# Optimization experiments

Hardware: AMD Instinct MI355X
Metric: run time of the kernel (lower is better)

## Reference

```python
import jax, jax.numpy as jnp
import numpy as np

B, T, C, H = 8, 2048, 1024, 64  # batch, seq_len(block_size), embedding_size, head_size


def setup_inputs() -> dict:
    key = jax.random.key(0)
    kx, kk, kq, kv = jax.random.split(key, 4)
    x = jax.random.normal(kx, (B, T, C), dtype=jnp.float32)
    # nn.Linear(C, H, bias=False) weights, stored as [in, out] for x @ W
    s = 1.0 / np.sqrt(C)
    Wk = jax.random.uniform(kk, (C, H), dtype=jnp.float32, minval=-s, maxval=s)
    Wq = jax.random.uniform(kq, (C, H), dtype=jnp.float32, minval=-s, maxval=s)
    Wv = jax.random.uniform(kv, (C, H), dtype=jnp.float32, minval=-s, maxval=s)
    return {"x": x, "Wk": Wk, "Wq": Wq, "Wv": Wv}


def reference(x, Wk, Wq, Wv):
    Bx, Tx, Cx = x.shape
    k = jnp.einsum('btc,ch->bth', x, Wk)
    q = jnp.einsum('btc,ch->bth', x, Wq)
    v = jnp.einsum('btc,ch->bth', x, Wv)
    # NOTE: original scales by embedding dim C ** -0.5, not head_size
    scores = jnp.einsum('bth,bsh->bts', q, k) * (Cx ** -0.5)  # [B,T,T]
    causal = jnp.tril(jnp.ones((Tx, Tx), dtype=bool))
    scores = jnp.where(causal, scores, -jnp.inf)
    attn = jax.nn.softmax(scores, axis=-1)
    # dropout is identity in eval/deterministic mode
    out = jnp.einsum('bts,bsh->bth', attn, v)  # [B,T,H]
    return out
```

## Files before the change

kernel.cpp:

```cpp
#include <hip/hip_runtime.h>
#include <hip/hip_bf16.h>
#include <math.h>


#define BT 16384
#define TSEQ 2048
#define XST 72

typedef __attribute__((ext_vector_type(8))) __bf16 bf16x8;
typedef __attribute__((ext_vector_type(8))) unsigned short ushort8;
typedef __attribute__((ext_vector_type(4))) float floatx4;

#define MFMA16(a, b, c) __builtin_amdgcn_mfma_f32_16x16x32_bf16( \
    __builtin_bit_cast(bf16x8, (a)), __builtin_bit_cast(bf16x8, (b)), (c), 0, 0, 0)

__device__ inline unsigned short f2bf(float f) {
  unsigned u = __builtin_bit_cast(unsigned, f);
  u += 0x7FFFu + ((u >> 16) & 1u);
  return (unsigned short)(u >> 16);
}
__device__ inline float bf2f(unsigned short s) {
  return __builtin_bit_cast(float, (unsigned)s << 16);
}
__device__ inline unsigned long long pack4bf(floatx4 f) {
  return (unsigned long long)f2bf(f[0]) | ((unsigned long long)f2bf(f[1]) << 16) |
         ((unsigned long long)f2bf(f[2]) << 32) | ((unsigned long long)f2bf(f[3]) << 48);
}
__device__ inline ushort8 pack8bf(floatx4 a, floatx4 b) {
  ushort8 t;
#pragma unroll
  for (int i = 0; i < 4; ++i) t[i] = f2bf(a[i]);
#pragma unroll
  for (int i = 0; i < 4; ++i) t[4 + i] = f2bf(b[i]);
  return t;
}
__device__ inline void glds16(const unsigned short* g, unsigned short* l) {
  __builtin_amdgcn_global_load_lds(
      (const __attribute__((address_space(1))) unsigned int*)g,
      (__attribute__((address_space(3))) unsigned int*)l, 16, 0, 0);
}

__global__ __launch_bounds__(256) void wt2_kernel(
    const float* __restrict__ Wq, const float* __restrict__ Wk,
    const float* __restrict__ Wv, unsigned short* __restrict__ Wt2) {
  __shared__ float ls[64][65];
  const int m = blockIdx.x >> 4;
  const int kci = blockIdx.x & 15;
  const int c0 = kci << 6;
  const float* __restrict__ W = (m == 0) ? Wq : (m == 1) ? Wk : Wv;
  const int tid = threadIdx.x;
#pragma unroll
  for (int i = 0; i < 16; ++i) {
    int idx = tid + (i << 8);
    int cl = idx >> 6, h = idx & 63;
    ls[cl][h] = W[(c0 + cl) * 64 + h];
  }
  __syncthreads();
  const int w = tid >> 6, lane = tid & 63;
  const int quad = lane >> 4, l16 = lane & 15;
  const int nt = (m << 2) + w;
#pragma unroll
  for (int half = 0; half < 2; ++half) {
    ushort8 t;
#pragma unroll
    for (int j = 0; j < 8; ++j)
      t[j] = f2bf(ls[(half << 5) + (quad << 3) + j][(w << 4) + l16]);
    *(ushort8*)(Wt2 + ((size_t)(((nt << 4) + kci) * 2 + half) << 9) +
                (lane << 3)) = t;
  }
}

#define XBS 4608
#define BB0 9216
#define BBS 12288

__global__ __launch_bounds__(512) void qkv_mfma(
    const float* __restrict__ x, const unsigned short* __restrict__ Wt2,
    unsigned short* __restrict__ Qf, unsigned short* __restrict__ Kf,
    unsigned short* __restrict__ Vf) {
  __shared__ __align__(16) unsigned short smem[46080];

  const int tid = threadIdx.x;
  const int w = tid >> 6, lane = tid & 63;
  const int quad = lane >> 4, l16 = lane & 15;
  const int wr = w >> 2, wn = w & 3;
  const int r0 = blockIdx.x << 6;
  const int xrow = (w << 3) + (lane >> 3);
  const int xcol = (lane & 7) << 3;
  const float* __restrict__ xp = x + (size_t)(r0 + xrow) * 1024 + xcol;
  const int xw_u16 = xrow * XST + xcol;

  floatx4 acc[2][3];
#pragma unroll
  for (int rt = 0; rt < 2; ++rt)
#pragma unroll
    for (int n = 0; n < 3; ++n) acc[rt][n] = (floatx4){0.f, 0.f, 0.f, 0.f};

  floatx4 pf[2][2];
  pf[0][0] = *(const floatx4*)(xp);
  pf[0][1] = *(const floatx4*)(xp + 4);
  __builtin_amdgcn_sched_barrier(0);
#pragma unroll
  for (int i = 0; i < 3; ++i) {
    const int f = 3 * w + i;
    glds16(Wt2 + ((size_t)(((f >> 1) << 4) * 2 + (f & 1)) << 9) + (lane << 3),
           &smem[BB0 + (f << 9)]);
  }
  __builtin_amdgcn_sched_barrier(0);
  pf[1][0] = *(const floatx4*)(xp + 64);
  pf[1][1] = *(const floatx4*)(xp + 68);
  __builtin_amdgcn_sched_barrier(0);
#pragma unroll
  for (int i = 0; i < 3; ++i) {
    const int f = 3 * w + i;
    glds16(Wt2 + ((size_t)((((f >> 1) << 4) + 1) * 2 + (f & 1)) << 9) +
               (lane << 3),
           &smem[BB0 + BBS + (f << 9)]);
  }
  __builtin_amdgcn_sched_barrier(0);
  *(ushort8*)&smem[xw_u16] = pack8bf(pf[0][0], pf[0][1]);
  __builtin_amdgcn_sched_barrier(0);
  asm volatile("s_waitcnt vmcnt(5)");
  asm volatile("s_waitcnt lgkmcnt(0)");
  __builtin_amdgcn_sched_barrier(0);
  __builtin_amdgcn_s_barrier();
  __builtin_amdgcn_sched_barrier(0);

#pragma unroll
  for (int c = 0; c < 16; ++c) {
    if (c + 1 < 16)
      *(ushort8*)&smem[((c + 1) & 1) * XBS + xw_u16] =
          pack8bf(pf[(c + 1) & 1][0], pf[(c + 1) & 1][1]);
    __builtin_amdgcn_sched_barrier(0);
    if (c + 2 < 16) {
      pf[c & 1][0] = *(const floatx4*)(xp + ((c + 2) << 6));
      pf[c & 1][1] = *(const floatx4*)(xp + ((c + 2) << 6) + 4);
      __builtin_amdgcn_sched_barrier(0);
#pragma unroll
      for (int i = 0; i < 3; ++i) {
        const int f = 3 * w + i;
        glds16(Wt2 + ((size_t)((((f >> 1) << 4) + (c + 2)) * 2 + (f & 1)) << 9) +
                   (lane << 3),
               &smem[BB0 + ((c + 2) % 3) * BBS + (f << 9)]);
      }
    }
    __builtin_amdgcn_sched_barrier(0);

    ushort8 af[2][2];
#pragma unroll
    for (int rt = 0; rt < 2; ++rt)
#pragma unroll
      for (int h = 0; h < 2; ++h)
        af[rt][h] = *(const ushort8*)&smem[(c & 1) * XBS +
            ((wr << 5) + (rt << 4) + l16) * XST + (h << 5) + (quad << 3)];
    ushort8 bfr[3][2];
#pragma unroll
    for (int n = 0; n < 3; ++n)
#pragma unroll
      for (int h = 0; h < 2; ++h)
        bfr[n][h] = *(const ushort8*)&smem[BB0 + (c % 3) * BBS +
            ((((3 * wn + n) << 1) + h) << 9) + (lane << 3)];
#pragma unroll
    for (int h = 0; h < 2; ++h)
#pragma unroll
      for (int rt = 0; rt < 2; ++rt)
#pragma unroll
        for (int n = 0; n < 3; ++n)
          acc[rt][n] = MFMA16(af[rt][h], bfr[n][h], acc[rt][n]);

    __builtin_amdgcn_sched_barrier(0);
    if (c < 14) { asm volatile("s_waitcnt vmcnt(5)"); }
    else        { asm volatile("s_waitcnt vmcnt(0)"); }
    asm volatile("s_waitcnt lgkmcnt(0)");
    __builtin_amdgcn_sched_barrier(0);
    __builtin_amdgcn_s_barrier();
    __builtin_amdgcn_sched_barrier(0);
  }

#pragma unroll
  for (int n = 0; n < 3; ++n) {
    const int nt = 3 * wn + n;
    const int m = nt >> 2, hg = nt & 3;
#pragma unroll
    for (int rt = 0; rt < 2; ++rt) {
      const int rowb = (wr << 5) + (rt << 4) + (quad << 2);
      if (m < 2) {
#pragma unroll
        for (int r = 0; r < 4; ++r)
          smem[m * XBS + (rowb + r) * XST + (hg << 4) + l16] =
              f2bf(acc[rt][n][r]);
      } else {
        *(unsigned long long*)&smem[2 * XBS + ((hg << 4) + l16) * XST + rowb] =
            pack4bf(acc[rt][n]);
      }
    }
  }
  __syncthreads();

  const int b = blockIdx.x >> 5, st = blockIdx.x & 31;
#pragma unroll
  for (int i = 0; i < 3; ++i) {
    const int f = w * 3 + i;
    const int m = f >> 3, idx = f & 7, grp = idx >> 1, kh = idx & 1;
    ushort8 t = *(const ushort8*)&smem[m * XBS + ((grp << 4) + l16) * XST +
                                       (kh << 5) + (quad << 3)];
    unsigned short* dst;
    if (m == 0)
      dst = Qf + (((size_t)(b * 128 + (st << 2) + grp) * 2 + kh) << 9);
    else if (m == 1)
      dst = Kf + (((size_t)((b * 32 + st) * 4 + grp) * 2 + kh) << 9);
    else
      dst = Vf + (((size_t)((b * 32 + st) * 4 + grp) * 2 + kh) << 9);
    *(ushort8*)(dst + (lane << 3)) = t;
  }
}

__global__ __launch_bounds__(256, 3) void attn_part(
    const unsigned short* __restrict__ Qf, const unsigned short* __restrict__ Kf,
    const unsigned short* __restrict__ Vf, float* __restrict__ part) {
  __shared__ __align__(16) unsigned short KV[2][8192];
  __shared__ unsigned short Pw[4][16 * XST];

  const int tid = threadIdx.x;
  const int w = tid >> 6, lane = tid & 63;
  const int quad = lane >> 4, l16 = lane & 15;
  const int b = blockIdx.x / 144;
  const int e = blockIdx.x - b * 144;
  int g = 0;
#pragma unroll
  for (int gg = 1; gg < 8; ++gg) g += (e >= 2 * gg * (gg + 1)) ? 1 : 0;
  const int rem2 = e - 2 * g * (g + 1);
  const int qt = (g << 2) + rem2 / (g + 1);
  const int ch = rem2 - (rem2 / (g + 1)) * (g + 1);
  const int s0 = ch << 2;
  const int s1 = (s0 + 4 < qt + 1) ? s0 + 4 : qt + 1;
  const int r16 = (qt << 2) + w;

#define KVIDX(ss, nt, kh) \
  (((((size_t)(b * 32 + (ss)) << 2) + (nt)) * 2 + (kh)) << 9)
#define STAGE_KV(ss, db)                                                     \
  {                                                                          \
    _Pragma("unroll") for (int r_ = 0; r_ < 4; ++r_) {                       \
      const int f_ = (r_ << 2) + w;                                          \
      const unsigned short* src_ =                                           \
          (f_ < 8) ? Kf + KVIDX(ss, (f_ >> 1), (f_ & 1)) + (lane << 3)       \
                   : Vf + KVIDX(ss, (f_ >> 1) - 4, (f_ & 1)) + (lane << 3);  \
      glds16(src_, &KV[db][f_ << 9]);                                        \
    }                                                                        \
  }

  const unsigned short* qbase =
      Qf + ((((size_t)b * 128 + r16) * 2) << 9) + (lane << 3);
  ushort8 qf0 = *(const ushort8*)qbase;
  ushort8 qf1 = *(const ushort8*)(qbase + 512);
  __builtin_amdgcn_sched_barrier(0);

  STAGE_KV(s0, 0);
  __builtin_amdgcn_sched_barrier(0);
  STAGE_KV((s0 + 1 < s1) ? s0 + 1 : s1 - 1, 1);
  __builtin_amdgcn_sched_barrier(0);
  asm volatile("s_waitcnt vmcnt(4)");
  __builtin_amdgcn_sched_barrier(0);
  __builtin_amdgcn_s_barrier();
  __builtin_amdgcn_sched_barrier(0);

  floatx4 acc[4], lacc;
#pragma unroll
  for (int nt = 0; nt < 4; ++nt) acc[nt] = (floatx4){0.f, 0.f, 0.f, 0.f};
  lacc = (floatx4){0.f, 0.f, 0.f, 0.f};
  const ushort8 ones = {0x3F80, 0x3F80, 0x3F80, 0x3F80,
                        0x3F80, 0x3F80, 0x3F80, 0x3F80};

  for (int s = s0; s < s1; ++s) {
    const int cur = (s - s0) & 1;
    ushort8 bk[4][2], bv[4][2];
#pragma unroll
    for (int nt = 0; nt < 4; ++nt)
#pragma unroll
      for (int kh = 0; kh < 2; ++kh) {
        bk[nt][kh] = *(const ushort8*)&KV[cur][((((nt << 1) + kh)) << 9) +
                                              (lane << 3)];
        bv[nt][kh] = *(const ushort8*)&KV[cur][(((8 + (nt << 1) + kh)) << 9) +
                                              (lane << 3)];
      }
    asm volatile("s_waitcnt lgkmcnt(0)");
    __builtin_amdgcn_sched_barrier(0);
    __builtin_amdgcn_s_barrier();
    __builtin_amdgcn_sched_barrier(0);

    STAGE_KV((s + 2 < s1) ? s + 2 : s1 - 1, cur);
    __builtin_amdgcn_sched_barrier(0);

    floatx4 sf[4];
#pragma unroll
    for (int nt = 0; nt < 4; ++nt) {
      sf[nt] = (floatx4){0.f, 0.f, 0.f, 0.f};
      sf[nt] = MFMA16(qf0, bk[nt][0], sf[nt]);
      sf[nt] = MFMA16(qf1, bk[nt][1], sf[nt]);
    }

    const bool diag = (s == qt);
    const int qrow = (w << 4) + (quad << 2);
#pragma unroll
    for (int nt = 0; nt < 4; ++nt) {
      const int keyl = (nt << 4) + l16;
#pragma unroll
      for (int r = 0; r < 4; ++r) {
        float ev = __expf(sf[nt][r] * 0.03125f);
        if (diag && keyl > qrow + r) ev = 0.f;
        Pw[w][((quad << 2) + r) * XST + keyl] = f2bf(ev);
      }
    }

#pragma unroll
    for (int kh = 0; kh < 2; ++kh) {
      ushort8 pa = *(const ushort8*)&Pw[w][l16 * XST + (kh << 5) + (quad << 3)];
      lacc = MFMA16(pa, ones, lacc);
#pragma unroll
      for (int nt = 0; nt < 4; ++nt) acc[nt] = MFMA16(pa, bv[nt][kh], acc[nt]);
    }

    __builtin_amdgcn_sched_barrier(0);
    asm volatile("s_waitcnt vmcnt(4)");
    __builtin_amdgcn_sched_barrier(0);
    __builtin_amdgcn_s_barrier();
    __builtin_amdgcn_sched_barrier(0);
  }
#undef STAGE_KV
#undef KVIDX

  float* slot = part + (size_t)(b * 144 + e) * 2112;
  if (l16 == 0) {
#pragma unroll
    for (int r = 0; r < 4; ++r) slot[(w << 4) + (quad << 2) + r] = lacc[r];
  }
  unsigned short* op = (unsigned short*)(slot + 64);
#pragma unroll
  for (int nt = 0; nt < 4; ++nt)
#pragma unroll
    for (int r = 0; r < 4; ++r)
      op[((w << 4) + (quad << 2) + r) * 64 + (nt << 4) + l16] = f2bf(acc[nt][r]);
}

__global__ __launch_bounds__(256) void attn_combine(
    const float* __restrict__ part, float* __restrict__ out) {
  const int rh = blockIdx.x & 1;
  const int bqt = blockIdx.x >> 1;
  const int b = bqt >> 5, qt = bqt & 31;
  const int tid = threadIdx.x;
  const int row = (rh << 5) + (tid >> 3);
  const int hseg = (tid & 7) << 3;
  const int g = qt >> 2;
  const int nch = g + 1;
  const int ebase = 2 * g * (g + 1) + (qt & 3) * (g + 1);

  float l = 0.f;
  float ov[8];
#pragma unroll
  for (int i = 0; i < 8; ++i) ov[i] = 0.f;
  for (int c = 0; c < nch; ++c) {
    const float* slot = part + (size_t)(b * 144 + ebase + c) * 2112;
    l += slot[row];
    ushort8 o0 = *(const ushort8*)((const unsigned short*)(slot + 64) +
                                   row * 64 + hseg);
#pragma unroll
    for (int i = 0; i < 8; ++i) ov[i] += bf2f(o0[i]);
  }
  const float inv = 1.f / l;
  float* o = out + ((size_t)(b * TSEQ + (qt << 6) + row)) * 64 + hseg;
#pragma unroll
  for (int i = 0; i < 8; ++i) o[i] = ov[i] * inv;
}

extern "C" void kernel_launch(void* const* d_in, const int* in_sizes, int n_in,
                              void* d_out, int out_size, void* d_ws, size_t ws_size,
                              hipStream_t stream) {
  const float* x  = (const float*)d_in[0];
  const float* Wk = (const float*)d_in[1];
  const float* Wq = (const float*)d_in[2];
  const float* Wv = (const float*)d_in[3];

  unsigned short* Qfw = (unsigned short*)d_ws;
  unsigned short* Kfw = Qfw + (size_t)BT * 64;
  unsigned short* Vfw = Kfw + (size_t)BT * 64;
  unsigned short* Wt2 = Vfw + (size_t)BT * 64;
  float* part = (float*)(Wt2 + 3 * 64 * 1024);

  wt2_kernel<<<48, 256, 0, stream>>>(Wq, Wk, Wv, Wt2);
  qkv_mfma<<<256, 512, 0, stream>>>(x, Wt2, Qfw, Kfw, Vfw);
  attn_part<<<1152, 256, 0, stream>>>(Qfw, Kfw, Vfw, part);
  attn_combine<<<512, 256, 0, stream>>>(part, (float*)d_out);
}
```

Measured before the change: 130.7 us.

## Shrink QKV projection tiles to 16 rows and load weights directly into registers

The QKV projection kernel moves from 64-row tiles on 256 blocks of 512 threads to 16-row tiles on 1024 blocks of 256 threads. Weight fragments are now loaded straight from global memory into registers and double-buffered, instead of being staged through LDS with global_load_lds. LDS use drops sharply and occupancy rises, so the 256 CUs get more work and latency is hidden better. In exchange, each weight fragment is reloaded by four times as many blocks, which raises L2 traffic, and the V-transpose store path becomes more complicated.

```diff
diff --git a/kernel.cpp b/kernel.cpp
--- a/kernel.cpp
+++ b/kernel.cpp
@@ -25,14 +25,6 @@
 __device__ inline unsigned long long pack4bf(floatx4 f) {
   return (unsigned long long)f2bf(f[0]) | ((unsigned long long)f2bf(f[1]) << 16) |
          ((unsigned long long)f2bf(f[2]) << 32) | ((unsigned long long)f2bf(f[3]) << 48);
-}
-__device__ inline ushort8 pack8bf(floatx4 a, floatx4 b) {
-  ushort8 t;
-#pragma unroll
-  for (int i = 0; i < 4; ++i) t[i] = f2bf(a[i]);
-#pragma unroll
-  for (int i = 0; i < 4; ++i) t[4 + i] = f2bf(b[i]);
-  return t;
 }
 __device__ inline void glds16(const unsigned short* g, unsigned short* l) {
   __builtin_amdgcn_global_load_lds(
@@ -70,148 +62,121 @@
   }
 }
 
-#define XBS 4608
-#define BB0 9216
-#define BBS 12288
-
-__global__ __launch_bounds__(512) void qkv_mfma(
+#define XB16 1152
+
+__global__ __launch_bounds__(256, 4) void qkv_mfma(
     const float* __restrict__ x, const unsigned short* __restrict__ Wt2,
     unsigned short* __restrict__ Qf, unsigned short* __restrict__ Kf,
     unsigned short* __restrict__ Vf) {
-  __shared__ __align__(16) unsigned short smem[46080];
+  __shared__ __align__(16) unsigned short smem[3840];
 
   const int tid = threadIdx.x;
   const int w = tid >> 6, lane = tid & 63;
   const int quad = lane >> 4, l16 = lane & 15;
-  const int wr = w >> 2, wn = w & 3;
-  const int r0 = blockIdx.x << 6;
-  const int xrow = (w << 3) + (lane >> 3);
-  const int xcol = (lane & 7) << 3;
+  const int r0 = blockIdx.x << 4;
+  const int xrow = tid >> 4;
+  const int xcol = (tid & 15) << 2;
   const float* __restrict__ xp = x + (size_t)(r0 + xrow) * 1024 + xcol;
-  const int xw_u16 = xrow * XST + xcol;
-
-  floatx4 acc[2][3];
-#pragma unroll
-  for (int rt = 0; rt < 2; ++rt)
-#pragma unroll
-    for (int n = 0; n < 3; ++n) acc[rt][n] = (floatx4){0.f, 0.f, 0.f, 0.f};
-
-  floatx4 pf[2][2];
-  pf[0][0] = *(const floatx4*)(xp);
-  pf[0][1] = *(const floatx4*)(xp + 4);
-  __builtin_amdgcn_sched_barrier(0);
+  const int xw = xrow * XST + xcol;
+  const unsigned short* __restrict__ bbase = Wt2 + (lane << 3);
+
+  floatx4 acc[3];
+#pragma unroll
+  for (int n = 0; n < 3; ++n) acc[n] = (floatx4){0.f, 0.f, 0.f, 0.f};
+
+  floatx4 pf[4];
+#pragma unroll
+  for (int s = 0; s < 4; ++s) pf[s] = *(const floatx4*)(xp + (s << 6));
+  ushort8 bfr[2][3][2];
+#pragma unroll
+  for (int n = 0; n < 3; ++n)
+#pragma unroll
+    for (int h = 0; h < 2; ++h)
+      bfr[0][n][h] = *(const ushort8*)(bbase +
+          ((size_t)(((3 * w + n) << 5) + h) << 9));
+  *(unsigned long long*)&smem[xw] = pack4bf(pf[0]);
+  asm volatile("s_waitcnt lgkmcnt(0)" ::: "memory");
+  __builtin_amdgcn_sched_barrier(0);
+  __builtin_amdgcn_s_barrier();
+  __builtin_amdgcn_sched_barrier(0);
+
+#pragma unroll
+  for (int c = 0; c < 16; ++c) {
+    const int cur = c & 1;
+    if (c + 1 < 16)
+      *(unsigned long long*)&smem[((c + 1) & 1) * XB16 + xw] =
+          pack4bf(pf[(c + 1) & 3]);
+    if (c + 4 < 16) pf[c & 3] = *(const floatx4*)(xp + ((c + 4) << 6));
+    if (c + 1 < 16) {
+#pragma unroll
+      for (int n = 0; n < 3; ++n)
+#pragma unroll
+        for (int h = 0; h < 2; ++h)
+          bfr[(c + 1) & 1][n][h] = *(const ushort8*)(bbase +
+              ((size_t)((((3 * w + n) << 4) + (c + 1)) * 2 + h) << 9));
+    }
+    ushort8 af[2];
+#pragma unroll
+    for (int h = 0; h < 2; ++h)
+      af[h] = *(const ushort8*)&smem[cur * XB16 + l16 * XST + (h << 5) +
+                                     (quad << 3)];
+#pragma unroll
+    for (int h = 0; h < 2; ++h)
+#pragma unroll
+      for (int n = 0; n < 3; ++n)
+        acc[n] = MFMA16(af[h], bfr[cur][n][h], acc[n]);
+
+    asm volatile("s_waitcnt lgkmcnt(0)" ::: "memory");
+    __builtin_amdgcn_sched_barrier(0);
+    __builtin_amdgcn_s_barrier();
+    __builtin_amdgcn_sched_barrier(0);
+  }
+
 #pragma unroll
   for (int i = 0; i < 3; ++i) {
-    const int f = 3 * w + i;
-    glds16(Wt2 + ((size_t)(((f >> 1) << 4) * 2 + (f & 1)) << 9) + (lane << 3),
-           &smem[BB0 + (f << 9)]);
-  }
-  __builtin_amdgcn_sched_barrier(0);
-  pf[1][0] = *(const floatx4*)(xp + 64);
-  pf[1][1] = *(const floatx4*)(xp + 68);
-  __builtin_amdgcn_sched_barrier(0);
-#pragma unroll
-  for (int i = 0; i < 3; ++i) {
-    const int f = 3 * w + i;
-    glds16(Wt2 + ((size_t)((((f >> 1) << 4) + 1) * 2 + (f & 1)) << 9) +
-               (lane << 3),
-           &smem[BB0 + BBS + (f << 9)]);
-  }
-  __builtin_amdgcn_sched_barrier(0);
-  *(ushort8*)&smem[xw_u16] = pack8bf(pf[0][0], pf[0][1]);
-  __builtin_amdgcn_sched_barrier(0);
-  asm volatile("s_waitcnt vmcnt(5)");
-  asm volatile("s_waitcnt lgkmcnt(0)");
-  __builtin_amdgcn_sched_barrier(0);
-  __builtin_amdgcn_s_barrier();
-  __builtin_amdgcn_sched_barrier(0);
-
-#pragma unroll
-  for (int c = 0; c < 16; ++c) {
-    if (c + 1 < 16)
-      *(ushort8*)&smem[((c + 1) & 1) * XBS + xw_u16] =
-          pack8bf(pf[(c + 1) & 1][0], pf[(c + 1) & 1][1]);
-    __builtin_amdgcn_sched_barrier(0);
-    if (c + 2 < 16) {
-      pf[c & 1][0] = *(const floatx4*)(xp + ((c + 2) << 6));
-      pf[c & 1][1] = *(const floatx4*)(xp + ((c + 2) << 6) + 4);
-      __builtin_amdgcn_sched_barrier(0);
-#pragma unroll
-      for (int i = 0; i < 3; ++i) {
-        const int f = 3 * w + i;
-        glds16(Wt2 + ((size_t)((((f >> 1) << 4) + (c + 2)) * 2 + (f & 1)) << 9) +
-                   (lane << 3),
-               &smem[BB0 + ((c + 2) % 3) * BBS + (f << 9)]);
+    const int nt = 3 * w + i;
+    const int m = nt >> 2, hg = nt & 3;
+    if (m < 2) {
+#pragma unroll
+      for (int r = 0; r < 4; ++r)
+        smem[m * XB16 + ((quad << 2) + r) * XST + (hg << 4) + l16] =
+            f2bf(acc[i][r]);
+    } else {
+      *(unsigned long long*)&smem[2304 + ((hg << 4) + l16) * 24 + (quad << 2)] =
+          pack4bf(acc[i]);
+    }
+  }
+  __syncthreads();
+
+  const int b = r0 >> 11;
+  const int r16 = (r0 & 2047) >> 4;
+  const int st = (r0 & 2047) >> 6;
+  const int ntK = (r0 >> 4) & 3;
+  const int khV = (r0 >> 5) & 1;
+  const int q0v = (r0 >> 3) & 3;
+#pragma unroll
+  for (int i = 0; i < 2; ++i) {
+    const int f = (w << 1) + i;
+    if (f < 2) {
+      const int kh = f;
+      ushort8 t = *(const ushort8*)&smem[l16 * XST + (kh << 5) + (quad << 3)];
+      *(ushort8*)(Qf + ((((size_t)b * 128 + r16) * 2 + kh) << 9) +
+                  (lane << 3)) = t;
+    } else if (f < 4) {
+      const int kh = f - 2;
+      ushort8 t = *(const ushort8*)&smem[XB16 + l16 * XST + (kh << 5) +
+                                         (quad << 3)];
+      *(ushort8*)(Kf + ((((size_t)(b * 32 + st) * 4 + ntK) * 2 + kh) << 9) +
+                  (lane << 3)) = t;
+    } else {
+      const int ntE = f - 4;
+      if ((quad >> 1) == (q0v >> 1)) {
+        ushort8 t = *(const ushort8*)&smem[2304 + ((ntE << 4) + l16) * 24 +
+                                           ((quad - q0v) << 3)];
+        *(ushort8*)(Vf + ((((size_t)(b * 32 + st) * 4 + ntE) * 2 + khV) << 9) +
+                    (lane << 3)) = t;
       }
     }
-    __builtin_amdgcn_sched_barrier(0);
-
-    ushort8 af[2][2];
-#pragma unroll
-    for (int rt = 0; rt < 2; ++rt)
-#pragma unroll
-      for (int h = 0; h < 2; ++h)
-        af[rt][h] = *(const ushort8*)&smem[(c & 1) * XBS +
-            ((wr << 5) + (rt << 4) + l16) * XST + (h << 5) + (quad << 3)];
-    ushort8 bfr[3][2];
-#pragma unroll
-    for (int n = 0; n < 3; ++n)
-#pragma unroll
-      for (int h = 0; h < 2; ++h)
-        bfr[n][h] = *(const ushort8*)&smem[BB0 + (c % 3) * BBS +
-            ((((3 * wn + n) << 1) + h) << 9) + (lane << 3)];
-#pragma unroll
-    for (int h = 0; h < 2; ++h)
-#pragma unroll
-      for (int rt = 0; rt < 2; ++rt)
-#pragma unroll
-        for (int n = 0; n < 3; ++n)
-          acc[rt][n] = MFMA16(af[rt][h], bfr[n][h], acc[rt][n]);
-
-    __builtin_amdgcn_sched_barrier(0);
-    if (c < 14) { asm volatile("s_waitcnt vmcnt(5)"); }
-    else        { asm volatile("s_waitcnt vmcnt(0)"); }
-    asm volatile("s_waitcnt lgkmcnt(0)");
-    __builtin_amdgcn_sched_barrier(0);
-    __builtin_amdgcn_s_barrier();
-    __builtin_amdgcn_sched_barrier(0);
-  }
-
-#pragma unroll
-  for (int n = 0; n < 3; ++n) {
-    const int nt = 3 * wn + n;
-    const int m = nt >> 2, hg = nt & 3;
-#pragma unroll
-    for (int rt = 0; rt < 2; ++rt) {
-      const int rowb = (wr << 5) + (rt << 4) + (quad << 2);
-      if (m < 2) {
-#pragma unroll
-        for (int r = 0; r < 4; ++r)
-          smem[m * XBS + (rowb + r) * XST + (hg << 4) + l16] =
-              f2bf(acc[rt][n][r]);
-      } else {
-        *(unsigned long long*)&smem[2 * XBS + ((hg << 4) + l16) * XST + rowb] =
-            pack4bf(acc[rt][n]);
-      }
-    }
-  }
-  __syncthreads();
-
-  const int b = blockIdx.x >> 5, st = blockIdx.x & 31;
-#pragma unroll
-  for (int i = 0; i < 3; ++i) {
-    const int f = w * 3 + i;
-    const int m = f >> 3, idx = f & 7, grp = idx >> 1, kh = idx & 1;
-    ushort8 t = *(const ushort8*)&smem[m * XBS + ((grp << 4) + l16) * XST +
-                                       (kh << 5) + (quad << 3)];
-    unsigned short* dst;
-    if (m == 0)
-      dst = Qf + (((size_t)(b * 128 + (st << 2) + grp) * 2 + kh) << 9);
-    else if (m == 1)
-      dst = Kf + (((size_t)((b * 32 + st) * 4 + grp) * 2 + kh) << 9);
-    else
-      dst = Vf + (((size_t)((b * 32 + st) * 4 + grp) * 2 + kh) << 9);
-    *(ushort8*)(dst + (lane << 3)) = t;
   }
 }
 
@@ -387,7 +352,7 @@
   float* part = (float*)(Wt2 + 3 * 64 * 1024);
 
   wt2_kernel<<<48, 256, 0, stream>>>(Wq, Wk, Wv, Wt2);
-  qkv_mfma<<<256, 512, 0, stream>>>(x, Wt2, Qfw, Kfw, Vfw);
+  qkv_mfma<<<1024, 256, 0, stream>>>(x, Wt2, Qfw, Kfw, Vfw);
   attn_part<<<1152, 256, 0, stream>>>(Qfw, Kfw, Vfw, part);
   attn_combine<<<512, 256, 0, stream>>>(part, (float*)d_out);
 }
```

Result: slower. 139.8 us (+7.0%).

## Split QKV projection into per-matrix blocks with XCD-aware row grouping

Applied to the files above, without the earlier changes.

The QKV projection kernel now launches 768 blocks of 256 threads instead of 256 blocks of 512, with each block computing only one of Q, K or V for a 64-row tile. Block indices are remapped so the three blocks sharing an x row tile land on the same XCD, which should help L2 reuse of x. This gives more blocks for occupancy across CUs and a smaller LDS footprint, and the x prefetch pipeline deepens to three stages. The cost is that each x tile is read from global memory three times instead of once.

```diff
diff --git a/kernel.cpp b/kernel.cpp
--- a/kernel.cpp
+++ b/kernel.cpp
@@ -70,57 +70,63 @@
   }
 }
 
-#define XBS 4608
-#define BB0 9216
-#define BBS 12288
-
-__global__ __launch_bounds__(512) void qkv_mfma(
+#define XQB 4608
+#define BQ0 9216
+#define BQS 4096
+
+__global__ __launch_bounds__(256, 3) void qkv_mfma(
     const float* __restrict__ x, const unsigned short* __restrict__ Wt2,
     unsigned short* __restrict__ Qf, unsigned short* __restrict__ Kf,
     unsigned short* __restrict__ Vf) {
-  __shared__ __align__(16) unsigned short smem[46080];
+  __shared__ __align__(16) unsigned short smem[21504];
 
   const int tid = threadIdx.x;
   const int w = tid >> 6, lane = tid & 63;
   const int quad = lane >> 4, l16 = lane & 15;
-  const int wr = w >> 2, wn = w & 3;
-  const int r0 = blockIdx.x << 6;
-  const int xrow = (w << 3) + (lane >> 3);
-  const int xcol = (lane & 7) << 3;
-  const float* __restrict__ xp = x + (size_t)(r0 + xrow) * 1024 + xcol;
-  const int xw_u16 = xrow * XST + xcol;
-
-  floatx4 acc[2][3];
-#pragma unroll
-  for (int rt = 0; rt < 2; ++rt)
-#pragma unroll
-    for (int n = 0; n < 3; ++n) acc[rt][n] = (floatx4){0.f, 0.f, 0.f, 0.f};
-
-  floatx4 pf[2][2];
-  pf[0][0] = *(const floatx4*)(xp);
-  pf[0][1] = *(const floatx4*)(xp + 4);
-  __builtin_amdgcn_sched_barrier(0);
-#pragma unroll
-  for (int i = 0; i < 3; ++i) {
-    const int f = 3 * w + i;
-    glds16(Wt2 + ((size_t)(((f >> 1) << 4) * 2 + (f & 1)) << 9) + (lane << 3),
-           &smem[BB0 + (f << 9)]);
-  }
-  __builtin_amdgcn_sched_barrier(0);
-  pf[1][0] = *(const floatx4*)(xp + 64);
-  pf[1][1] = *(const floatx4*)(xp + 68);
-  __builtin_amdgcn_sched_barrier(0);
-#pragma unroll
-  for (int i = 0; i < 3; ++i) {
-    const int f = 3 * w + i;
-    glds16(Wt2 + ((size_t)((((f >> 1) << 4) + 1) * 2 + (f & 1)) << 9) +
+  const int xcd = blockIdx.x & 7, idx = blockIdx.x >> 3;
+  const int rg = (xcd << 5) + idx / 3;
+  const int mm = idx - (idx / 3) * 3;
+  const int r0 = rg << 6;
+
+  const int xrow = tid >> 2;
+  const int xcs = (tid & 3) << 4;
+  const float* __restrict__ xp = x + (size_t)(r0 + xrow) * 1024 + xcs;
+  const int xw = xrow * XST + xcs;
+
+  floatx4 acc[4];
+#pragma unroll
+  for (int n = 0; n < 4; ++n) acc[n] = (floatx4){0.f, 0.f, 0.f, 0.f};
+
+  floatx4 pf[3][4];
+
+#pragma unroll
+  for (int i = 0; i < 2; ++i) {
+    const int f = (w << 1) + i;
+    glds16(Wt2 + ((size_t)((((mm << 2) + (f >> 1)) * 16 + 0) * 2 + (f & 1)) << 9) +
                (lane << 3),
-           &smem[BB0 + BBS + (f << 9)]);
-  }
-  __builtin_amdgcn_sched_barrier(0);
-  *(ushort8*)&smem[xw_u16] = pack8bf(pf[0][0], pf[0][1]);
-  __builtin_amdgcn_sched_barrier(0);
-  asm volatile("s_waitcnt vmcnt(5)");
+           &smem[BQ0 + (f << 9)]);
+  }
+  __builtin_amdgcn_sched_barrier(0);
+#pragma unroll
+  for (int p = 0; p < 4; ++p) pf[0][p] = *(const floatx4*)(xp + (p << 2));
+  __builtin_amdgcn_sched_barrier(0);
+#pragma unroll
+  for (int i = 0; i < 2; ++i) {
+    const int f = (w << 1) + i;
+    glds16(Wt2 + ((size_t)((((mm << 2) + (f >> 1)) * 16 + 1) * 2 + (f & 1)) << 9) +
+               (lane << 3),
+           &smem[BQ0 + BQS + (f << 9)]);
+  }
+  __builtin_amdgcn_sched_barrier(0);
+#pragma unroll
+  for (int p = 0; p < 4; ++p) pf[1][p] = *(const floatx4*)(xp + 64 + (p << 2));
+#pragma unroll
+  for (int p = 0; p < 4; ++p) pf[2][p] = *(const floatx4*)(xp + 128 + (p << 2));
+  __builtin_amdgcn_sched_barrier(0);
+  *(ushort8*)&smem[xw] = pack8bf(pf[0][0], pf[0][1]);
+  *(ushort8*)&smem[xw + 8] = pack8bf(pf[0][2], pf[0][3]);
+  __builtin_amdgcn_sched_barrier(0);
+  asm volatile("s_waitcnt vmcnt(10)");
   asm volatile("s_waitcnt lgkmcnt(0)");
   __builtin_amdgcn_sched_barrier(0);
   __builtin_amdgcn_s_barrier();
@@ -128,89 +134,88 @@
 
 #pragma unroll
   for (int c = 0; c < 16; ++c) {
-    if (c + 1 < 16)
-      *(ushort8*)&smem[((c + 1) & 1) * XBS + xw_u16] =
-          pack8bf(pf[(c + 1) & 1][0], pf[(c + 1) & 1][1]);
+    const int cur = c & 1;
+    if (c + 1 < 16) {
+      *(ushort8*)&smem[((c + 1) & 1) * XQB + xw] =
+          pack8bf(pf[(c + 1) % 3][0], pf[(c + 1) % 3][1]);
+      *(ushort8*)&smem[((c + 1) & 1) * XQB + xw + 8] =
+          pack8bf(pf[(c + 1) % 3][2], pf[(c + 1) % 3][3]);
+    }
     __builtin_amdgcn_sched_barrier(0);
     if (c + 2 < 16) {
-      pf[c & 1][0] = *(const floatx4*)(xp + ((c + 2) << 6));
-      pf[c & 1][1] = *(const floatx4*)(xp + ((c + 2) << 6) + 4);
-      __builtin_amdgcn_sched_barrier(0);
-#pragma unroll
-      for (int i = 0; i < 3; ++i) {
-        const int f = 3 * w + i;
-        glds16(Wt2 + ((size_t)((((f >> 1) << 4) + (c + 2)) * 2 + (f & 1)) << 9) +
-                   (lane << 3),
-               &smem[BB0 + ((c + 2) % 3) * BBS + (f << 9)]);
+#pragma unroll
+      for (int i = 0; i < 2; ++i) {
+        const int f = (w << 1) + i;
+        glds16(Wt2 + ((size_t)((((mm << 2) + (f >> 1)) * 16 + (c + 2)) * 2 +
+                               (f & 1)) << 9) + (lane << 3),
+               &smem[BQ0 + ((c + 2) % 3) * BQS + (f << 9)]);
       }
     }
     __builtin_amdgcn_sched_barrier(0);
-
-    ushort8 af[2][2];
-#pragma unroll
-    for (int rt = 0; rt < 2; ++rt)
+    if (c + 3 < 16) {
+#pragma unroll
+      for (int p = 0; p < 4; ++p)
+        pf[(c + 3) % 3][p] = *(const floatx4*)(xp + ((c + 3) << 6) + (p << 2));
+    }
+    __builtin_amdgcn_sched_barrier(0);
+
+    ushort8 af[2];
+#pragma unroll
+    for (int h = 0; h < 2; ++h)
+      af[h] = *(const ushort8*)&smem[cur * XQB + ((w << 4) + l16) * XST +
+                                     (h << 5) + (quad << 3)];
+    ushort8 bfr[4][2];
+#pragma unroll
+    for (int n = 0; n < 4; ++n)
 #pragma unroll
       for (int h = 0; h < 2; ++h)
-        af[rt][h] = *(const ushort8*)&smem[(c & 1) * XBS +
-            ((wr << 5) + (rt << 4) + l16) * XST + (h << 5) + (quad << 3)];
-    ushort8 bfr[3][2];
-#pragma unroll
-    for (int n = 0; n < 3; ++n)
-#pragma unroll
-      for (int h = 0; h < 2; ++h)
-        bfr[n][h] = *(const ushort8*)&smem[BB0 + (c % 3) * BBS +
-            ((((3 * wn + n) << 1) + h) << 9) + (lane << 3)];
+        bfr[n][h] = *(const ushort8*)&smem[BQ0 + (c % 3) * BQS +
+                                           (((n << 1) + h) << 9) + (lane << 3)];
 #pragma unroll
     for (int h = 0; h < 2; ++h)
 #pragma unroll
-      for (int rt = 0; rt < 2; ++rt)
-#pragma unroll
-        for (int n = 0; n < 3; ++n)
-          acc[rt][n] = MFMA16(af[rt][h], bfr[n][h], acc[rt][n]);
-
-    __builtin_amdgcn_sched_barrier(0);
-    if (c < 14) { asm volatile("s_waitcnt vmcnt(5)"); }
-    else        { asm volatile("s_waitcnt vmcnt(0)"); }
+      for (int n = 0; n < 4; ++n)
+        acc[n] = MFMA16(af[h], bfr[n][h], acc[n]);
+
+    __builtin_amdgcn_sched_barrier(0);
+    if (c <= 12)      { asm volatile("s_waitcnt vmcnt(10)"); }
+    else if (c == 13) { asm volatile("s_waitcnt vmcnt(6)"); }
+    else              { asm volatile("s_waitcnt vmcnt(0)"); }
     asm volatile("s_waitcnt lgkmcnt(0)");
     __builtin_amdgcn_sched_barrier(0);
     __builtin_amdgcn_s_barrier();
     __builtin_amdgcn_sched_barrier(0);
   }
 
-#pragma unroll
-  for (int n = 0; n < 3; ++n) {
-    const int nt = 3 * wn + n;
-    const int m = nt >> 2, hg = nt & 3;
-#pragma unroll
-    for (int rt = 0; rt < 2; ++rt) {
-      const int rowb = (wr << 5) + (rt << 4) + (quad << 2);
-      if (m < 2) {
-#pragma unroll
-        for (int r = 0; r < 4; ++r)
-          smem[m * XBS + (rowb + r) * XST + (hg << 4) + l16] =
-              f2bf(acc[rt][n][r]);
-      } else {
-        *(unsigned long long*)&smem[2 * XBS + ((hg << 4) + l16) * XST + rowb] =
-            pack4bf(acc[rt][n]);
-      }
-    }
+  const int b = rg >> 5, st = rg & 31;
+  if (mm < 2) {
+#pragma unroll
+    for (int n = 0; n < 4; ++n)
+#pragma unroll
+      for (int r = 0; r < 4; ++r)
+        smem[((w << 4) + (quad << 2) + r) * XST + (n << 4) + l16] =
+            f2bf(acc[n][r]);
+  } else {
+#pragma unroll
+    for (int n = 0; n < 4; ++n)
+      *(unsigned long long*)&smem[((n << 4) + l16) * XST + (w << 4) +
+                                  (quad << 2)] = pack4bf(acc[n]);
   }
   __syncthreads();
 
-  const int b = blockIdx.x >> 5, st = blockIdx.x & 31;
-#pragma unroll
-  for (int i = 0; i < 3; ++i) {
-    const int f = w * 3 + i;
-    const int m = f >> 3, idx = f & 7, grp = idx >> 1, kh = idx & 1;
-    ushort8 t = *(const ushort8*)&smem[m * XBS + ((grp << 4) + l16) * XST +
-                                       (kh << 5) + (quad << 3)];
+#pragma unroll
+  for (int i = 0; i < 2; ++i) {
+    const int f = (w << 1) + i;
+    const int sub = f >> 1, kh = f & 1;
+    ushort8 t = *(const ushort8*)&smem[((sub << 4) + l16) * XST + (kh << 5) +
+                                       (quad << 3)];
     unsigned short* dst;
-    if (m == 0)
-      dst = Qf + (((size_t)(b * 128 + (st << 2) + grp) * 2 + kh) << 9);
-    else if (m == 1)
-      dst = Kf + (((size_t)((b * 32 + st) * 4 + grp) * 2 + kh) << 9);
+    if (mm == 0)
+      dst = Qf + ((((size_t)b * 128 + (st << 2) + sub) * 2 + kh) << 9);
+    else if (mm == 1)
+      dst = Kf + ((((size_t)(b * 32 + st) * 4 + sub) * 2 + kh) << 9);
     else
-      dst = Vf + (((size_t)((b * 32 + st) * 4 + grp) * 2 + kh) << 9);
+      dst = Vf + ((((size_t)(b * 32 + st) * 4 + sub) * 2 + kh) << 9);
     *(ushort8*)(dst + (lane << 3)) = t;
   }
 }
@@ -387,7 +392,7 @@
   float* part = (float*)(Wt2 + 3 * 64 * 1024);
 
   wt2_kernel<<<48, 256, 0, stream>>>(Wq, Wk, Wv, Wt2);
-  qkv_mfma<<<256, 512, 0, stream>>>(x, Wt2, Qfw, Kfw, Vfw);
+  qkv_mfma<<<768, 256, 0, stream>>>(x, Wt2, Qfw, Kfw, Vfw);
   attn_part<<<1152, 256, 0, stream>>>(Qfw, Kfw, Vfw, part);
   attn_combine<<<512, 256, 0, stream>>>(part, (float*)d_out);
 }
```

Measured after the change: 140.1 us. 1.07x slower.
